# Performance work log

Measured on AMD Instinct MI355X. Metric: run time of the kernel, lower is better.

## Reference

```python
import jax, jax.numpy as jnp
import numpy as np

NUM_HEADS = 16

def setup_inputs() -> dict:
    key = jax.random.key(0)
    k1, k2, k3 = jax.random.split(key, 3)
    B, T, D = 4, 2048, 1024
    x = jax.random.normal(k1, (B, T, D), dtype=jnp.float32)
    # lecun_normal: std = 1/sqrt(fan_in)
    w = jax.random.normal(k2, (3 * D, D), dtype=jnp.float32) * (1.0 / np.sqrt(D))
    w_out = jax.random.normal(k3, (D, D), dtype=jnp.float32) * (1.0 / np.sqrt(D))
    return {"x": x, "w": w, "w_out": w_out}


def reference(x, w, w_out):
    B, T, D = x.shape
    H = NUM_HEADS
    L = D // H
    # qkv projection: (B,T,3D)
    q, k, v = jnp.split(jnp.matmul(x, w.T), 3, axis=2)
    # -> (T,B,H,L) time-major for the scan
    q = q.reshape(B, T, H, L).transpose(1, 0, 2, 3)
    k = k.reshape(B, T, H, L).transpose(1, 0, 2, 3)
    v = v.reshape(B, T, H, L).transpose(1, 0, 2, 3)
    scale = jax.lax.rsqrt(jnp.float32(L))
    k_exp = jnp.exp(k * scale) + 1e-6            # (T,B,H,L)
    k_norm = jnp.cumsum(k_exp, axis=0)           # causal normalizer
    qs = jax.nn.softmax(q * scale, axis=-1) / k_norm

    def step(carry, args):
        qs_t, k_t, v_t = args                    # each (B,H,L)
        # accumulate outer product k_t v_t^T into (B,H,L,L) state
        carry = carry + k_t[..., :, None] * v_t[..., None, :]
        y_t = jnp.einsum('bhl,bhlm->bhm', qs_t, carry)
        return carry, y_t

    init = jnp.zeros((B, H, L, L), dtype=x.dtype)
    _, y = jax.lax.scan(step, init, (qs, k_exp, v))   # y: (T,B,H,L)
    y = y.reshape(T, B, D).transpose(1, 0, 2)         # (B,T,D)
    return jnp.matmul(y, w_out)                       # Dense, no bias
```

## Files before the change

### kernel.cpp

```cpp
#include <hip/hip_runtime.h>
#include <math.h>

#define Bsz   4
#define Tsz   2048
#define Dsz   1024
#define Hsz   16
#define Lsz   64
#define BHsz  64
#define CH    64
#define NCH   32
#define QKVLD 3072
#define SCL   0.125f
#define QSC   512.0f
#define QSCI  (1.0f/512.0f)

typedef float  floatx4 __attribute__((ext_vector_type(4)));
typedef _Float16 half8 __attribute__((ext_vector_type(8)));
typedef _Float16 half4 __attribute__((ext_vector_type(4)));
typedef _Float16 half2v __attribute__((ext_vector_type(2)));

#define AS1 __attribute__((address_space(1)))
#define AS3 __attribute__((address_space(3)))

static __device__ __forceinline__ void gload_lds16(const void* g, void* l) {
  __builtin_amdgcn_global_load_lds((const AS1 unsigned int*)g,
                                   (AS3 unsigned int*)l, 16, 0, 0);
}

static __device__ __forceinline__ float wave_max64(float v) {
#pragma unroll
  for (int off = 1; off < 64; off <<= 1) v = fmaxf(v, __shfl_xor(v, off));
  return v;
}
static __device__ __forceinline__ float wave_sum64(float v) {
#pragma unroll
  for (int off = 1; off < 64; off <<= 1) v += __shfl_xor(v, off);
  return v;
}

__launch_bounds__(256)
__global__ void prep(const float* __restrict__ x, _Float16* __restrict__ xh,
                     const float* __restrict__ w, _Float16* __restrict__ wh,
                     const float* __restrict__ wo, _Float16* __restrict__ woT) {
  const int blk = blockIdx.x, tid = threadIdx.x;
  if (blk < 11264) {
    const float* in  = (blk < 8192) ? x : w;
    _Float16*   outp = (blk < 8192) ? xh : wh;
    const int bi = (blk < 8192) ? blk : blk - 8192;
    const int i = (bi * 256 + tid) * 4;
    float4 v = *(const float4*)(in + i);
    half4 h = { (_Float16)v.x, (_Float16)v.y, (_Float16)v.z, (_Float16)v.w };
    *(half4*)(outp + i) = h;
  } else {
    __shared__ float tile[32][33];
    const int bi = blk - 11264;
    const int bx = (bi & 31) * 32;
    const int by = (bi >> 5) * 32;
    const int tx = tid & 31, ty0 = tid >> 5;
#pragma unroll
    for (int p = 0; p < 4; p++) {
      const int ty = ty0 + p * 8;
      tile[ty][tx] = wo[(size_t)(by + ty) * 1024 + bx + tx];
    }
    __syncthreads();
#pragma unroll
    for (int p = 0; p < 4; p++) {
      const int ty = ty0 + p * 8;
      woT[(size_t)(bx + ty) * 1024 + by + tx] = (_Float16)tile[tx][ty];
    }
  }
}

__launch_bounds__(256)
__global__ void gemm_f16_bt_f32(const _Float16* __restrict__ A, const _Float16* __restrict__ B,
                                float* __restrict__ C, int M, int N, int K) {
  __shared__ _Float16 As[128][32];
  __shared__ _Float16 Bs[128][32];
  const int tid  = threadIdx.x;
  const int wave = tid >> 6, lane = tid & 63;
  const int m0 = blockIdx.y * 128, n0 = blockIdx.x * 128;
  const int wm = (wave >> 1) * 64, wn = (wave & 1) * 64;
  const int fr = lane & 15;
  const int fq = lane >> 4;
  const int lr = lane >> 2;
  const int lk = (lane & 3) * 8;

  floatx4 zero = {0.f, 0.f, 0.f, 0.f};
  floatx4 acc[4][4];
#pragma unroll
  for (int mt = 0; mt < 4; mt++)
#pragma unroll
    for (int nt = 0; nt < 4; nt++) acc[mt][nt] = zero;

  for (int k0 = 0; k0 < K; k0 += 32) {
    __syncthreads();
#pragma unroll
    for (int j = 0; j < 2; j++) {
      const int ia = wave * 2 + j;
      gload_lds16(A + (size_t)(m0 + ia * 16 + lr) * K + k0 + lk, &As[ia * 16][0]);
      gload_lds16(B + (size_t)(n0 + ia * 16 + lr) * K + k0 + lk, &Bs[ia * 16][0]);
    }
    __syncthreads();

    half8 af[4], bf[4];
#pragma unroll
    for (int i = 0; i < 4; i++) {
      af[i] = *(const half8*)&As[wm + i * 16 + fr][fq * 8];
      bf[i] = *(const half8*)&Bs[wn + i * 16 + fr][fq * 8];
    }
#pragma unroll
    for (int mt = 0; mt < 4; mt++)
#pragma unroll
      for (int nt = 0; nt < 4; nt++)
        acc[mt][nt] = __builtin_amdgcn_mfma_f32_16x16x32_f16(af[mt], bf[nt], acc[mt][nt], 0, 0, 0);
  }
#pragma unroll
  for (int mt = 0; mt < 4; mt++)
#pragma unroll
    for (int nt = 0; nt < 4; nt++)
#pragma unroll
      for (int r = 0; r < 4; r++) {
        const int row = m0 + wm + mt * 16 + fq * 4 + r;
        const int col = n0 + wn + nt * 16 + fr;
        C[(size_t)row * N + col] = acc[mt][nt][r];
      }
}

__launch_bounds__(256)
__global__ void gemm_f16_bt_c16(const _Float16* __restrict__ A, const _Float16* __restrict__ B,
                                _Float16* __restrict__ C, int M, int N, int K) {
  __shared__ _Float16 As[128][32];
  __shared__ _Float16 Bs[128][32];
  const int tid  = threadIdx.x;
  const int wave = tid >> 6, lane = tid & 63;
  const int m0 = blockIdx.y * 128, n0 = blockIdx.x * 128;
  const int wm = (wave >> 1) * 64, wn = (wave & 1) * 64;
  const int fr = lane & 15;
  const int fq = lane >> 4;
  const int lr = lane >> 2;
  const int lk = (lane & 3) * 8;

  floatx4 zero = {0.f, 0.f, 0.f, 0.f};
  floatx4 acc[4][4];
#pragma unroll
  for (int mt = 0; mt < 4; mt++)
#pragma unroll
    for (int nt = 0; nt < 4; nt++) acc[mt][nt] = zero;

  for (int k0 = 0; k0 < K; k0 += 32) {
    __syncthreads();
#pragma unroll
    for (int j = 0; j < 2; j++) {
      const int ia = wave * 2 + j;
      gload_lds16(A + (size_t)(m0 + ia * 16 + lr) * K + k0 + lk, &As[ia * 16][0]);
      gload_lds16(B + (size_t)(n0 + ia * 16 + lr) * K + k0 + lk, &Bs[ia * 16][0]);
    }
    __syncthreads();

    half8 af[4], bf[4];
#pragma unroll
    for (int i = 0; i < 4; i++) {
      af[i] = *(const half8*)&As[wm + i * 16 + fr][fq * 8];
      bf[i] = *(const half8*)&Bs[wn + i * 16 + fr][fq * 8];
    }
#pragma unroll
    for (int mt = 0; mt < 4; mt++)
#pragma unroll
      for (int nt = 0; nt < 4; nt++)
        acc[mt][nt] = __builtin_amdgcn_mfma_f32_16x16x32_f16(af[mt], bf[nt], acc[mt][nt], 0, 0, 0);
  }
#pragma unroll
  for (int mt = 0; mt < 4; mt++)
#pragma unroll
    for (int nt = 0; nt < 4; nt++)
#pragma unroll
      for (int r = 0; r < 4; r++) {
        const int row = m0 + wm + mt * 16 + fq * 4 + r;
        const int col = n0 + wn + nt * 16 + fr;
        C[(size_t)row * N + col] = (_Float16)acc[mt][nt][r];
      }
}

__launch_bounds__(256)
__global__ void chunk_kv(const _Float16* __restrict__ qkv, float* __restrict__ KV,
                         float* __restrict__ Ksum) {
  const int blk = blockIdx.x;
  const int bh = blk >> 3, cgrp = blk & 7;
  const int b = bh >> 4, h = bh & 15;
  const int tid = threadIdx.x;
  const int wave = tid >> 6, lane = tid & 63;
  const int fr = lane & 15, fq = lane >> 4;
  const int m2  = (tid & 31) * 2;
  const int tg8 = (tid >> 5) * 8;

  __shared__ __align__(16) _Float16 KxT[64][72];
  __shared__ __align__(16) _Float16 VT [64][72];

  for (int cc = 0; cc < 4; cc++) {
    const int c = cgrp * 4 + cc;
    const size_t base = ((size_t)(b * Tsz + c * CH)) * QKVLD + h * 64;
    __syncthreads();
    half8 klo, khi, vlo, vhi;
#pragma unroll
    for (int j = 0; j < 8; j++) {
      const int t = tg8 + j;
      half2v kk = *(const half2v*)(qkv + base + (size_t)t * QKVLD + 1024 + m2);
      klo[j] = (_Float16)(expf((float)kk[0] * SCL) + 1e-6f);
      khi[j] = (_Float16)(expf((float)kk[1] * SCL) + 1e-6f);
      half2v vv = *(const half2v*)(qkv + base + (size_t)t * QKVLD + 2048 + m2);
      vlo[j] = vv[0]; vhi[j] = vv[1];
    }
    *(half8*)&KxT[m2][tg8]     = klo;
    *(half8*)&KxT[m2 + 1][tg8] = khi;
    *(half8*)&VT[m2][tg8]      = vlo;
    *(half8*)&VT[m2 + 1][tg8]  = vhi;
    __syncthreads();

    floatx4 acc[4];
#pragma unroll
    for (int j = 0; j < 4; j++) acc[j] = (floatx4){0.f, 0.f, 0.f, 0.f};
#pragma unroll
    for (int ks = 0; ks < 2; ks++) {
      half8 av = *(const half8*)&VT[wave * 16 + fr][ks * 32 + fq * 8];
#pragma unroll
      for (int j = 0; j < 4; j++) {
        half8 bv = *(const half8*)&KxT[j * 16 + fr][ks * 32 + fq * 8];
        acc[j] = __builtin_amdgcn_mfma_f32_16x16x32_f16(av, bv, acc[j], 0, 0, 0);
      }
    }
    float* KVp = KV + ((size_t)(bh * NCH + c)) * 4096;
#pragma unroll
    for (int j = 0; j < 4; j++)
#pragma unroll
      for (int r = 0; r < 4; r++)
        KVp[(wave * 16 + fq * 4 + r) * 64 + j * 16 + fr] = acc[j][r];

    if (tid < 64) {
      float s = 0.f;
      const half8* row = (const half8*)&KxT[tid][0];
#pragma unroll
      for (int j8 = 0; j8 < 8; j8++) {
        half8 v8 = row[j8];
#pragma unroll
        for (int j = 0; j < 8; j++) s += (float)v8[j];
      }
      Ksum[(bh * NCH + c) * 64 + tid] = s;
    }
  }
}

__launch_bounds__(256)
__global__ void prefix_kern(float* __restrict__ KV, float* __restrict__ Ksum) {
  const int tid = threadIdx.x;
  if (blockIdx.x < 1024) {
    const int bh = blockIdx.x >> 4;
    const int e  = (blockIdx.x & 15) * 256 + tid;
    float* p = KV + (size_t)bh * NCH * 4096 + e;
    float acc = 0.f;
#pragma unroll 4
    for (int c = 0; c < NCH; c++) {
      float t = p[(size_t)c * 4096];
      p[(size_t)c * 4096] = acc;
      acc += t;
    }
  } else {
    const int cid = (blockIdx.x - 1024) * 256 + tid;
    const int bh = cid >> 6, l = cid & 63;
    float* p = Ksum + bh * NCH * 64 + l;
    float acc = 0.f;
#pragma unroll 4
    for (int c = 0; c < NCH; c++) {
      float t = p[c * 64];
      p[c * 64] = acc;
      acc += t;
    }
  }
}

__launch_bounds__(256)
__global__ void chunk_y(const _Float16* __restrict__ qkv, const float* __restrict__ KV,
                        const float* __restrict__ Ksum, _Float16* __restrict__ Y) {
  const int bh = blockIdx.x, c = blockIdx.y;
  const int b = bh >> 4, h = bh & 15;
  const int tid = threadIdx.x;
  const int wave = tid >> 6, lane = tid & 63;

  __shared__ __align__(16) _Float16 kxh[64][72];
  __shared__ __align__(16) _Float16 kni[64][72];
  __shared__ __align__(16) _Float16 Ph[64][136];
  __shared__ __align__(16) _Float16 Bh[64][136];

  const size_t base = ((size_t)(b * Tsz + c * CH)) * QKVLD + h * 64;
  const float* KVp = KV + ((size_t)(bh * NCH + c)) * 4096;
  const int ksoff = (bh * NCH + c) * 64;

  _Float16 qreg[16];
#pragma unroll
  for (int i = 0; i < 16; i++)
    qreg[i] = qkv[base + (size_t)(wave * 16 + i) * QKVLD + lane];

  {
    const int rr  = tid >> 3;
    const int sg8 = (tid & 7) * 8;
#pragma unroll
    for (int p = 0; p < 2; p++) {
      const int t = p * 32 + rr;
      half8 kv = *(const half8*)(qkv + base + (size_t)t * QKVLD + 1024 + sg8);
      half8 kx16;
#pragma unroll
      for (int j = 0; j < 8; j++)
        kx16[j] = (_Float16)(expf((float)kv[j] * SCL) + 1e-6f);
      *(half8*)&kxh[t][sg8] = kx16;
    }
  }
  {
    const int m2  = (tid & 31) * 2;
    const int tg8 = (tid >> 5) * 8;
    half8 vlo, vhi;
#pragma unroll
    for (int j = 0; j < 8; j++) {
      const int t = tg8 + j;
      half2v vv = *(const half2v*)(qkv + base + (size_t)t * QKVLD + 2048 + m2);
      vlo[j] = vv[0]; vhi[j] = vv[1];
    }
    *(half8*)&Bh[m2][64 + tg8]     = vlo;
    *(half8*)&Bh[m2 + 1][64 + tg8] = vhi;
  }
  {
    const int m  = tid >> 2;
    const int l0 = (tid & 3) * 16;
#pragma unroll
    for (int q = 0; q < 2; q++) {
      float4 s0 = *(const float4*)(KVp + m * 64 + l0 + q * 8);
      float4 s1 = *(const float4*)(KVp + m * 64 + l0 + q * 8 + 4);
      half8 hh = { (_Float16)s0.x, (_Float16)s0.y, (_Float16)s0.z, (_Float16)s0.w,
                   (_Float16)s1.x, (_Float16)s1.y, (_Float16)s1.z, (_Float16)s1.w };
      *(half8*)&Bh[m][l0 + q * 8] = hh;
    }
  }
  __syncthreads();

#pragma unroll
  for (int i = 0; i < 16; i++) {
    const int l = wave * 16 + i;
    float v = (float)kxh[lane][l];
#pragma unroll
    for (int off = 1; off < 64; off <<= 1) {
      float n = __shfl_up(v, off);
      if (lane >= off) v += n;
    }
    kni[lane][l] = (_Float16)(QSC / (Ksum[ksoff + l] + v));
  }
  __syncthreads();

#pragma unroll
  for (int i = 0; i < 16; i++) {
    const int t = wave * 16 + i;
    float v = (float)qreg[i] * SCL;
    float m = wave_max64(v);
    float e = expf(v - m);
    float s = wave_sum64(e);
    Ph[t][lane] = (_Float16)((e / s) * (float)kni[t][lane]);
  }
  __syncthreads();

  const int wm = (wave >> 1) * 32, wn = (wave & 1) * 32;
  const int fr = lane & 15, fq = lane >> 4;
  {
    floatx4 zero = {0.f, 0.f, 0.f, 0.f};
    floatx4 a2[2][2];
#pragma unroll
    for (int mt = 0; mt < 2; mt++)
#pragma unroll
      for (int nt = 0; nt < 2; nt++) a2[mt][nt] = zero;
#pragma unroll
    for (int ks = 0; ks < 2; ks++) {
      half8 af[2], bf[2];
#pragma unroll
      for (int i = 0; i < 2; i++) {
        af[i] = *(const half8*)&Ph[wm + i * 16 + fr][ks * 32 + fq * 8];
        bf[i] = *(const half8*)&kxh[wn + i * 16 + fr][ks * 32 + fq * 8];
      }
#pragma unroll
      for (int mt = 0; mt < 2; mt++)
#pragma unroll
        for (int nt = 0; nt < 2; nt++)
          a2[mt][nt] = __builtin_amdgcn_mfma_f32_16x16x32_f16(af[mt], bf[nt], a2[mt][nt], 0, 0, 0);
    }
#pragma unroll
    for (int mt = 0; mt < 2; mt++)
#pragma unroll
      for (int nt = 0; nt < 2; nt++)
#pragma unroll
        for (int r = 0; r < 4; r++) {
          const int t = wm + mt * 16 + fq * 4 + r;
          const int s = wn + nt * 16 + fr;
          Ph[t][64 + s] = (_Float16)(s <= t ? a2[mt][nt][r] : 0.f);
        }
  }
  __syncthreads();

  {
    floatx4 zero = {0.f, 0.f, 0.f, 0.f};
    floatx4 acc[2][2];
#pragma unroll
    for (int mt = 0; mt < 2; mt++)
#pragma unroll
      for (int nt = 0; nt < 2; nt++) acc[mt][nt] = zero;
#pragma unroll
    for (int ks = 0; ks < 4; ks++) {
      half8 af[2], bf[2];
#pragma unroll
      for (int i = 0; i < 2; i++) {
        af[i] = *(const half8*)&Ph[wm + i * 16 + fr][ks * 32 + fq * 8];
        bf[i] = *(const half8*)&Bh[wn + i * 16 + fr][ks * 32 + fq * 8];
      }
#pragma unroll
      for (int mt = 0; mt < 2; mt++)
#pragma unroll
        for (int nt = 0; nt < 2; nt++)
          acc[mt][nt] = __builtin_amdgcn_mfma_f32_16x16x32_f16(af[mt], bf[nt], acc[mt][nt], 0, 0, 0);
    }
#pragma unroll
    for (int mt = 0; mt < 2; mt++)
#pragma unroll
      for (int nt = 0; nt < 2; nt++)
#pragma unroll
        for (int r = 0; r < 4; r++) {
          const int t = wm + mt * 16 + fq * 4 + r;
          const int m = wn + nt * 16 + fr;
          Y[(size_t)(b * Tsz + c * CH + t) * Dsz + h * 64 + m] =
              (_Float16)(acc[mt][nt][r] * QSCI);
        }
  }
}

extern "C" void kernel_launch(void* const* d_in, const int* in_sizes, int n_in,
                              void* d_out, int out_size, void* d_ws, size_t ws_size,
                              hipStream_t stream) {
  const float* x     = (const float*)d_in[0];
  const float* w     = (const float*)d_in[1];
  const float* w_out = (const float*)d_in[2];
  float* out = (float*)d_out;

  _Float16* xh   = (_Float16*)d_ws;
  _Float16* Yh   = xh;
  _Float16* wh   = xh + (size_t)8192 * 1024;
  _Float16* woT  = wh + (size_t)3072 * 1024;
  _Float16* qkvh = woT + (size_t)1024 * 1024;
  float* KV   = (float*)(qkvh + (size_t)8192 * 3072);
  float* Ksum = KV + (size_t)BHsz * NCH * 4096;

  prep<<<12288, 256, 0, stream>>>(x, xh, w, wh, w_out, woT);

  gemm_f16_bt_c16<<<dim3(24, 64), 256, 0, stream>>>(xh, wh, qkvh, 8192, 3072, 1024);

  chunk_kv<<<512, 256, 0, stream>>>(qkvh, KV, Ksum);
  prefix_kern<<<1040, 256, 0, stream>>>(KV, Ksum);
  chunk_y<<<dim3(BHsz, NCH), 256, 0, stream>>>(qkvh, KV, Ksum, Yh);

  gemm_f16_bt_f32<<<dim3(8, 64), 256, 0, stream>>>(Yh, woT, out, 8192, 1024, 1024);
}
```

Measured before the change: 262.6 us.

## Fuse exp(k) into QKV GEMM epilogue and use MFMA for in-chunk prefix sum

The QKV GEMM epilogue now applies exp(k*scale)+1e-6 to the K column range and stores it, so chunk_kv and chunk_y no longer compute the exponential themselves. In chunk_y, the per-column shuffle-based prefix sum over time is replaced by an MFMA product with a lower-triangular ones matrix. The Y output is staged through LDS so it can be written with 16-byte vector stores. This cuts duplicated transcendental work and shuffle-heavy scans, at the cost of storing k_exp in fp16 and using the faster __expf.

```diff
diff --git a/kernel.cpp b/kernel.cpp
--- a/kernel.cpp
+++ b/kernel.cpp
@@ -139,6 +139,7 @@
   const int fq = lane >> 4;
   const int lr = lane >> 2;
   const int lk = (lane & 3) * 8;
+  const bool kreg = (n0 >= 1024) && (n0 < 2048);
 
   floatx4 zero = {0.f, 0.f, 0.f, 0.f};
   floatx4 acc[4][4];
@@ -177,7 +178,9 @@
       for (int r = 0; r < 4; r++) {
         const int row = m0 + wm + mt * 16 + fq * 4 + r;
         const int col = n0 + wn + nt * 16 + fr;
-        C[(size_t)row * N + col] = (_Float16)acc[mt][nt][r];
+        float v = acc[mt][nt][r];
+        if (kreg) v = __expf(v * SCL) + 1e-6f;
+        C[(size_t)row * N + col] = (_Float16)v;
       }
 }
 
@@ -205,8 +208,7 @@
     for (int j = 0; j < 8; j++) {
       const int t = tg8 + j;
       half2v kk = *(const half2v*)(qkv + base + (size_t)t * QKVLD + 1024 + m2);
-      klo[j] = (_Float16)(expf((float)kk[0] * SCL) + 1e-6f);
-      khi[j] = (_Float16)(expf((float)kk[1] * SCL) + 1e-6f);
+      klo[j] = kk[0]; khi[j] = kk[1];
       half2v vv = *(const half2v*)(qkv + base + (size_t)t * QKVLD + 2048 + m2);
       vlo[j] = vv[0]; vhi[j] = vv[1];
     }
@@ -284,9 +286,10 @@
   const int b = bh >> 4, h = bh & 15;
   const int tid = threadIdx.x;
   const int wave = tid >> 6, lane = tid & 63;
+  const int fr = lane & 15, fq = lane >> 4;
 
   __shared__ __align__(16) _Float16 kxh[64][72];
-  __shared__ __align__(16) _Float16 kni[64][72];
+  __shared__ __align__(16) _Float16 kxT[64][72];
   __shared__ __align__(16) _Float16 Ph[64][136];
   __shared__ __align__(16) _Float16 Bh[64][136];
 
@@ -299,30 +302,34 @@
   for (int i = 0; i < 16; i++)
     qreg[i] = qkv[base + (size_t)(wave * 16 + i) * QKVLD + lane];
 
+  float ksb[4];
+#pragma unroll
+  for (int j = 0; j < 4; j++) ksb[j] = Ksum[ksoff + j * 16 + fr];
+
   {
     const int rr  = tid >> 3;
     const int sg8 = (tid & 7) * 8;
 #pragma unroll
     for (int p = 0; p < 2; p++) {
       const int t = p * 32 + rr;
-      half8 kv = *(const half8*)(qkv + base + (size_t)t * QKVLD + 1024 + sg8);
-      half8 kx16;
-#pragma unroll
-      for (int j = 0; j < 8; j++)
-        kx16[j] = (_Float16)(expf((float)kv[j] * SCL) + 1e-6f);
-      *(half8*)&kxh[t][sg8] = kx16;
+      *(half8*)&kxh[t][sg8] =
+          *(const half8*)(qkv + base + (size_t)t * QKVLD + 1024 + sg8);
     }
   }
   {
     const int m2  = (tid & 31) * 2;
     const int tg8 = (tid >> 5) * 8;
-    half8 vlo, vhi;
+    half8 klo, khi, vlo, vhi;
 #pragma unroll
     for (int j = 0; j < 8; j++) {
       const int t = tg8 + j;
+      half2v kk = *(const half2v*)(qkv + base + (size_t)t * QKVLD + 1024 + m2);
+      klo[j] = kk[0]; khi[j] = kk[1];
       half2v vv = *(const half2v*)(qkv + base + (size_t)t * QKVLD + 2048 + m2);
       vlo[j] = vv[0]; vhi[j] = vv[1];
     }
+    *(half8*)&kxT[m2][tg8]         = klo;
+    *(half8*)&kxT[m2 + 1][tg8]     = khi;
     *(half8*)&Bh[m2][64 + tg8]     = vlo;
     *(half8*)&Bh[m2 + 1][64 + tg8] = vhi;
   }
@@ -340,39 +347,50 @@
   }
   __syncthreads();
 
-#pragma unroll
-  for (int i = 0; i < 16; i++) {
-    const int l = wave * 16 + i;
-    float v = (float)kxh[lane][l];
-#pragma unroll
-    for (int off = 1; off < 64; off <<= 1) {
-      float n = __shfl_up(v, off);
-      if (lane >= off) v += n;
-    }
-    kni[lane][l] = (_Float16)(QSC / (Ksum[ksoff + l] + v));
-  }
-  __syncthreads();
+  {
+    floatx4 kacc[4];
+#pragma unroll
+    for (int j = 0; j < 4; j++) kacc[j] = (floatx4){0.f, 0.f, 0.f, 0.f};
+#pragma unroll
+    for (int ks = 0; ks < 2; ks++) {
+      half8 af;
+#pragma unroll
+      for (int j = 0; j < 8; j++)
+        af[j] = (ks * 32 + fq * 8 + j) <= (wave * 16 + fr) ? (_Float16)1.0f
+                                                           : (_Float16)0.0f;
+#pragma unroll
+      for (int j = 0; j < 4; j++) {
+        half8 bf = *(const half8*)&kxT[j * 16 + fr][ks * 32 + fq * 8];
+        kacc[j] = __builtin_amdgcn_mfma_f32_16x16x32_f16(af, bf, kacc[j], 0, 0, 0);
+      }
+    }
+    __syncthreads();
+#pragma unroll
+    for (int j = 0; j < 4; j++)
+#pragma unroll
+      for (int r = 0; r < 4; r++)
+        kxT[wave * 16 + fq * 4 + r][j * 16 + fr] =
+            (_Float16)(QSC / (ksb[j] + kacc[j][r]));
+  }
 
 #pragma unroll
   for (int i = 0; i < 16; i++) {
     const int t = wave * 16 + i;
     float v = (float)qreg[i] * SCL;
     float m = wave_max64(v);
-    float e = expf(v - m);
+    float e = __expf(v - m);
     float s = wave_sum64(e);
-    Ph[t][lane] = (_Float16)((e / s) * (float)kni[t][lane]);
+    Ph[t][lane] = (_Float16)((e / s) * (float)kxT[t][lane]);
   }
   __syncthreads();
 
   const int wm = (wave >> 1) * 32, wn = (wave & 1) * 32;
-  const int fr = lane & 15, fq = lane >> 4;
-  {
-    floatx4 zero = {0.f, 0.f, 0.f, 0.f};
+  {
     floatx4 a2[2][2];
 #pragma unroll
     for (int mt = 0; mt < 2; mt++)
 #pragma unroll
-      for (int nt = 0; nt < 2; nt++) a2[mt][nt] = zero;
+      for (int nt = 0; nt < 2; nt++) a2[mt][nt] = (floatx4){0.f, 0.f, 0.f, 0.f};
 #pragma unroll
     for (int ks = 0; ks < 2; ks++) {
       half8 af[2], bf[2];
@@ -401,12 +419,11 @@
   __syncthreads();
 
   {
-    floatx4 zero = {0.f, 0.f, 0.f, 0.f};
     floatx4 acc[2][2];
 #pragma unroll
     for (int mt = 0; mt < 2; mt++)
 #pragma unroll
-      for (int nt = 0; nt < 2; nt++) acc[mt][nt] = zero;
+      for (int nt = 0; nt < 2; nt++) acc[mt][nt] = (floatx4){0.f, 0.f, 0.f, 0.f};
 #pragma unroll
     for (int ks = 0; ks < 4; ks++) {
       half8 af[2], bf[2];
@@ -426,12 +443,17 @@
 #pragma unroll
       for (int nt = 0; nt < 2; nt++)
 #pragma unroll
-        for (int r = 0; r < 4; r++) {
-          const int t = wm + mt * 16 + fq * 4 + r;
-          const int m = wn + nt * 16 + fr;
-          Y[(size_t)(b * Tsz + c * CH + t) * Dsz + h * 64 + m] =
+        for (int r = 0; r < 4; r++)
+          kxh[wm + mt * 16 + fq * 4 + r][wn + nt * 16 + fr] =
               (_Float16)(acc[mt][nt][r] * QSCI);
-        }
+  }
+  __syncthreads();
+
+  {
+    const int ty = tid >> 2, sg = (tid & 3) * 16;
+    _Float16* yrow = Y + (size_t)(b * Tsz + c * CH + ty) * Dsz + h * 64 + sg;
+    *(half8*)(yrow)     = *(const half8*)&kxh[ty][sg];
+    *(half8*)(yrow + 8) = *(const half8*)&kxh[ty][sg + 8];
   }
 }
 
```

New measurement: 257.8 us. Within noise of the previous version (-1.8%).
